# Performance work log

Hardware: AMD Instinct MI355X
Metric: run time of the kernel (lower is better)

The kernel has to match this reference:

```python
import jax, jax.numpy as jnp
import numpy as np

B, S, D, H = 2, 2048, 1024, 16
HD = D // H  # head_dim = 64


def setup_inputs() -> dict:
    key = jax.random.key(0)
    ks = jax.random.split(key, 12)
    scale = 1.0 / np.sqrt(D)
    inp = {
        "query": jax.random.normal(ks[0], (B, S, D), dtype=jnp.float32),
        "key_in": jax.random.normal(ks[1], (B, S, D), dtype=jnp.float32),
        "value": jax.random.normal(ks[2], (B, S, D), dtype=jnp.float32),
        "mask": jnp.zeros((B, S), dtype=bool),
        # nn.Linear weights stored as [out, in] like torch; y = x @ W.T + b
        "Wq": jax.random.normal(ks[3], (D, D), dtype=jnp.float32) * scale,
        "bq": jnp.zeros((D,), dtype=jnp.float32),
        "Wk": jax.random.normal(ks[4], (D, D), dtype=jnp.float32) * scale,
        "bk": jnp.zeros((D,), dtype=jnp.float32),
        "Wv": jax.random.normal(ks[5], (D, D), dtype=jnp.float32) * scale,
        "bv": jnp.zeros((D,), dtype=jnp.float32),
        "Wo": jax.random.normal(ks[6], (D, D), dtype=jnp.float32) * scale,
        "bo": jnp.zeros((D,), dtype=jnp.float32),
    }
    return inp


def reference(query, key_in, value, mask, Wq, bq, Wk, bk, Wv, bv, Wo, bo):
    def split_heads(x):  # [B,S,D] -> [B,H,S,HD]
        return x.reshape(B, -1, H, HD).transpose(0, 2, 1, 3)

    Q = split_heads(query @ Wq.T + bq)
    K = split_heads(key_in @ Wk.T + bk)
    V = split_heads(value @ Wv.T + bv)

    scores = jnp.einsum("bhqd,bhkd->bhqk", Q, K) / np.sqrt(HD)
    # key-padding mask: True -> -inf, broadcast over heads and query positions
    scores = jnp.where(mask[:, None, None, :], -jnp.inf, scores)
    attn = jax.nn.softmax(scores, axis=-1)
    out = jnp.einsum("bhqk,bhkd->bhqd", attn, V)  # [B,H,S,HD]
    out = out.transpose(0, 2, 1, 3).reshape(B, -1, D)
    return out @ Wo.T + bo
```

## Files before the change

### kernel.cpp

```cpp
#include <hip/hip_runtime.h>

typedef __attribute__((ext_vector_type(8))) __bf16 bf16x8;
typedef __attribute__((ext_vector_type(4))) float f32x4;
typedef __attribute__((ext_vector_type(16))) float f32x16;
typedef __attribute__((ext_vector_type(4))) unsigned int u32x4;
typedef __attribute__((ext_vector_type(8))) _Float16 f16x8;
typedef __attribute__((ext_vector_type(4))) _Float16 f16x4;
typedef unsigned short us;

#define SEQ 2048
#define DIM 1024
#define NH 16
#define HDIM 64

#define QSCALE 0.1803368801111204f

__device__ inline us f2bf(float f) {
    unsigned u = __builtin_bit_cast(unsigned, f);
    u += 0x7FFFu + ((u >> 16) & 1u);
    return (us)(u >> 16);
}

__device__ inline unsigned sx32(unsigned v) {
    return (unsigned)__shfl_xor((int)v, 32);
}

__device__ __forceinline__ void gload16(const us* g, us* l) {
    __builtin_amdgcn_global_load_lds(
        (const __attribute__((address_space(1))) unsigned int*)(const void*)g,
        (__attribute__((address_space(3))) unsigned int*)(void*)l, 16, 0, 0);
}

__global__ __launch_bounds__(256) void cast_many(
    const float* __restrict__ s0, const float* __restrict__ s1,
    const float* __restrict__ s2, const float* __restrict__ s3,
    us* __restrict__ dst, int n_each)
{
    const float* src = (blockIdx.y == 0) ? s0 : (blockIdx.y == 1) ? s1
                     : (blockIdx.y == 2) ? s2 : s3;
    size_t base = (size_t)blockIdx.y * (size_t)n_each;
    int i = (blockIdx.x * 256 + threadIdx.x) * 4;
    if (i < n_each) {
        float4 v = *(const float4*)(src + i);
        ushort4 o;
        o.x = f2bf(v.x); o.y = f2bf(v.y); o.z = f2bf(v.z); o.w = f2bf(v.w);
        *(ushort4*)(dst + base + i) = o;
    }
}

__global__ __launch_bounds__(64) void maskpack(
    const unsigned char* __restrict__ mask, unsigned* __restrict__ mw)
{
    int t = blockIdx.x * 64 + threadIdx.x;
    unsigned wv = 0;
#pragma unroll
    for (int j = 0; j < 32; j++) wv |= (mask[t * 32 + j] ? 1u : 0u) << j;
    mw[t] = wv;
}

#define BM 128
#define BN 128
#define BK 64

__device__ __forceinline__ void gemm_core(
    const us* __restrict__ A, const us* __restrict__ W,
    const float* __restrict__ bias, void* __restrict__ out,
    int M, int N, int K, int mode, float oscale)
{
    __shared__ us lA[BM * BK];
    __shared__ us lB[BN * BK];

    const int tid  = threadIdx.x;
    const int lane = tid & 63;
    const int w    = tid >> 6;
    const int wm   = w >> 1, wn = w & 1;
    const int m0   = blockIdx.y * BM, n0 = blockIdx.x * BN;
    const int g    = lane >> 4, li = lane & 15;

    const f32x4 fz = {0.f, 0.f, 0.f, 0.f};
    f32x4 acc[4][4];
#pragma unroll
    for (int i = 0; i < 4; i++)
#pragma unroll
        for (int j = 0; j < 4; j++) acc[i][j] = fz;

    for (int k0 = 0; k0 < K; k0 += BK) {
#pragma unroll
        for (int i = 0; i < 4; i++) {
            int v = tid + i * 256;
            int row = v >> 3, c8 = (v & 7) * 8;
            gload16(&A[(size_t)(m0 + row) * K + k0 + c8], &lA[v * 8]);
            gload16(&W[(size_t)(n0 + row) * K + k0 + c8], &lB[v * 8]);
        }
        __syncthreads();
#pragma unroll
        for (int kk = 0; kk < 2; kk++) {
            bf16x8 af[4], bfr[4];
#pragma unroll
            for (int i = 0; i < 4; i++)
                af[i] = *(const bf16x8*)&lA[(wm * 64 + i * 16 + li) * BK + kk * 32 + g * 8];
#pragma unroll
            for (int j = 0; j < 4; j++)
                bfr[j] = *(const bf16x8*)&lB[(wn * 64 + j * 16 + li) * BK + kk * 32 + g * 8];
#pragma unroll
            for (int i = 0; i < 4; i++)
#pragma unroll
                for (int j = 0; j < 4; j++)
                    acc[i][j] = __builtin_amdgcn_mfma_f32_16x16x32_bf16(
                        af[i], bfr[j], acc[i][j], 0, 0, 0);
        }
        __syncthreads();
    }

    const int r0 = g * 4;
#pragma unroll
    for (int i = 0; i < 4; i++) {
#pragma unroll
        for (int j = 0; j < 4; j++) {
            int col = n0 + wn * 64 + j * 16 + li;
            float bs = bias[col];
#pragma unroll
            for (int r = 0; r < 4; r++) {
                int row = m0 + wm * 64 + i * 16 + r0 + r;
                float val = (acc[i][j][r] + bs) * oscale;
                if (mode == 2) {
                    ((float*)out)[(size_t)row * N + col] = val;
                } else {
                    int b = row >> 11, s = row & (SEQ - 1);
                    int h = col >> 6, hd = col & (HDIM - 1);
                    size_t idx = (mode == 0)
                        ? ((((size_t)b * NH + h) * SEQ + s) * HDIM + hd)
                        : ((((size_t)b * NH + h) * HDIM + hd) * SEQ + s);
                    ((us*)out)[idx] = f2bf(val);
                }
            }
        }
    }
}

__global__ __launch_bounds__(256) void gemm_qkv(
    const us* __restrict__ xq, const us* __restrict__ xk, const us* __restrict__ xv,
    const us* __restrict__ wq, const us* __restrict__ wk, const us* __restrict__ wv,
    const float* __restrict__ bq, const float* __restrict__ bk, const float* __restrict__ bv,
    us* __restrict__ Qb, us* __restrict__ Kb, us* __restrict__ VTb)
{
    int z = blockIdx.z;
    if (z == 0)      gemm_core(xq, wq, bq, Qb,  2 * SEQ, DIM, DIM, 0, QSCALE);
    else if (z == 1) gemm_core(xk, wk, bk, Kb,  2 * SEQ, DIM, DIM, 0, 1.0f);
    else             gemm_core(xv, wv, bv, VTb, 2 * SEQ, DIM, DIM, 1, 1.0f);
}

__global__ __launch_bounds__(256) void gemm_one(
    const us* __restrict__ A, const us* __restrict__ W,
    const float* __restrict__ bias, float* __restrict__ out)
{
    gemm_core(A, W, bias, out, 2 * SEQ, DIM, DIM, 2, 1.0f);
}

__global__ __launch_bounds__(256, 4) void attn_split(
    const us* __restrict__ Qb, const us* __restrict__ Kb,
    const us* __restrict__ VT, const unsigned* __restrict__ mw,
    _Float16* __restrict__ opart, float* __restrict__ mlpart)
{
    const int tid  = threadIdx.x;
    const int w    = tid >> 6, lane = tid & 63;
    const int unit = blockIdx.x * 4 + w;
    const int tile = unit >> 1, half = unit & 1;
    const int bh   = tile >> 6, qt = tile & 63;
    const int b    = bh >> 4;
    const int q0   = qt * 32;
    const int ql   = lane & 31, hi = lane >> 5;
    const int kv0  = half * 1024, kv1 = kv0 + 1024;

    const us* Qp  = Qb + (((size_t)bh * SEQ) + q0 + ql) * HDIM + hi * 8;
    const us* Kp  = Kb + ((size_t)bh * SEQ + ql) * HDIM + hi * 8;
    const us* Vp0 = VT + ((size_t)bh * HDIM + ql) * SEQ + hi * 8;
    const us* Vp1 = Vp0 + 32 * SEQ;

    bf16x8 qf[4];
#pragma unroll
    for (int t = 0; t < 4; t++) qf[t] = *(const bf16x8*)(Qp + t * 16);

    const f32x16 z16 = {0,0,0,0,0,0,0,0,0,0,0,0,0,0,0,0};
    f32x16 o0 = z16, o1 = z16;
    float mrun = -1e30f, lrun = 0.f;

    bf16x8 kf[4];
#pragma unroll
    for (int t = 0; t < 4; t++) kf[t] = *(const bf16x8*)(Kp + (size_t)kv0 * HDIM + t * 16);

    for (int kv = kv0; kv < kv1; kv += 32) {
        f32x16 s = z16;
#pragma unroll
        for (int t = 0; t < 4; t++)
            s = __builtin_amdgcn_mfma_f32_32x32x16_bf16(kf[t], qf[t], s, 0, 0, 0);

        if (kv + 32 < kv1) {
            const us* Kn = Kp + (size_t)(kv + 32) * HDIM;
#pragma unroll
            for (int t = 0; t < 4; t++) kf[t] = *(const bf16x8*)(Kn + t * 16);
        }
        bf16x8 vf0[2], vf1[2];
#pragma unroll
        for (int t = 0; t < 2; t++) {
            vf0[t] = *(const bf16x8*)(Vp0 + kv + t * 16);
            vf1[t] = *(const bf16x8*)(Vp1 + kv + t * 16);
        }

        unsigned m32 = (unsigned)__builtin_amdgcn_readfirstlane(
            (int)mw[b * 64 + (kv >> 5)]);

        float t8[8];
#pragma unroll
        for (int j = 0; j < 8; j++) t8[j] = fmaxf(s[j], s[j + 8]);
#pragma unroll
        for (int j = 0; j < 4; j++) t8[j] = fmaxf(t8[j], t8[j + 4]);
        float pmax = fmaxf(fmaxf(t8[0], t8[1]), fmaxf(t8[2], t8[3]));

        if (!__all(pmax <= mrun + 8.f)) {
            float pm = fmaxf(pmax, __shfl_xor(pmax, 32));
            float nm = fmaxf(mrun, pm);
            float corr = __builtin_amdgcn_exp2f(mrun - nm);
            lrun *= corr;
#pragma unroll
            for (int j = 0; j < 16; j++) { o0[j] *= corr; o1[j] *= corr; }
            mrun = nm;
        }

        float p[16];
#pragma unroll
        for (int r = 0; r < 16; r++) p[r] = __builtin_amdgcn_exp2f(s[r] - mrun);
        if (m32) {
            unsigned ms = hi ? (m32 >> 4) : m32;
#pragma unroll
            for (int r = 0; r < 16; r++)
                if ((ms >> ((r & 3) + 8 * (r >> 2))) & 1) p[r] = 0.f;
        }
        float a8[8];
#pragma unroll
        for (int j = 0; j < 8; j++) a8[j] = p[j] + p[j + 8];
#pragma unroll
        for (int j = 0; j < 4; j++) a8[j] += a8[j + 4];
        lrun += (a8[0] + a8[1]) + (a8[2] + a8[3]);

        unsigned pw[8];
#pragma unroll
        for (int j = 0; j < 8; j++)
            asm("v_cvt_pk_bf16_f32 %0, %1, %2"
                : "=v"(pw[j]) : "v"(p[2 * j]), "v"(p[2 * j + 1]));

        unsigned y0 = sx32(hi ? pw[0] : pw[2]);
        unsigned y1 = sx32(hi ? pw[1] : pw[3]);
        unsigned y2 = sx32(hi ? pw[4] : pw[6]);
        unsigned y3 = sx32(hi ? pw[5] : pw[7]);

        u32x4 t0, t1;
        t0.x = hi ? y0    : pw[0];
        t0.y = hi ? y1    : pw[1];
        t0.z = hi ? pw[2] : y0;
        t0.w = hi ? pw[3] : y1;
        t1.x = hi ? y2    : pw[4];
        t1.y = hi ? y3    : pw[5];
        t1.z = hi ? pw[6] : y2;
        t1.w = hi ? pw[7] : y3;
        bf16x8 pa0 = __builtin_bit_cast(bf16x8, t0);
        bf16x8 pa1 = __builtin_bit_cast(bf16x8, t1);

        o0 = __builtin_amdgcn_mfma_f32_32x32x16_bf16(vf0[0], pa0, o0, 0, 0, 0);
        o0 = __builtin_amdgcn_mfma_f32_32x32x16_bf16(vf0[1], pa1, o0, 0, 0, 0);
        o1 = __builtin_amdgcn_mfma_f32_32x32x16_bf16(vf1[0], pa0, o1, 0, 0, 0);
        o1 = __builtin_amdgcn_mfma_f32_32x32x16_bf16(vf1[1], pa1, o1, 0, 0, 0);
    }

    float lh  = lrun + __shfl_xor(lrun, 32);
    float inv = __builtin_amdgcn_rcpf(lh);

    size_t orow = (size_t)half * 65536 + (size_t)bh * SEQ + q0 + ql;
    _Float16* od = opart + orow * 64;
#pragma unroll
    for (int g2 = 0; g2 < 4; g2++) {
        f16x4 v0, v1;
#pragma unroll
        for (int j = 0; j < 4; j++) {
            v0[j] = (_Float16)(o0[4 * g2 + j] * inv);
            v1[j] = (_Float16)(o1[4 * g2 + j] * inv);
        }
        *(f16x4*)(od + 8 * g2 + 4 * hi)      = v0;
        *(f16x4*)(od + 32 + 8 * g2 + 4 * hi) = v1;
    }
    if (hi == 0) {
        float2 mlv; mlv.x = mrun; mlv.y = lh;
        *(float2*)&mlpart[orow * 2] = mlv;
    }
}

__global__ __launch_bounds__(256) void attn_combine(
    const _Float16* __restrict__ op, const float* __restrict__ ml,
    us* __restrict__ AO)
{
    int t   = blockIdx.x * 256 + threadIdx.x;
    int row = t >> 3, dc = (t & 7) * 8;
    int bh  = row >> 11, q = row & (SEQ - 1);
    int b   = bh >> 4, h = bh & 15;

    float2 ml0 = *(const float2*)&ml[(size_t)row * 2];
    float2 ml1 = *(const float2*)&ml[(size_t)(65536 + row) * 2];
    float M  = fmaxf(ml0.x, ml1.x);
    float w0 = ml0.y * __builtin_amdgcn_exp2f(ml0.x - M);
    float w1 = ml1.y * __builtin_amdgcn_exp2f(ml1.x - M);
    float wi = __builtin_amdgcn_rcpf(w0 + w1);
    float a0 = w0 * wi, a1 = w1 * wi;

    f16x8 v0 = *(const f16x8*)(op + (size_t)row * 64 + dc);
    f16x8 v1 = *(const f16x8*)(op + 4194304 + (size_t)row * 64 + dc);

    ushort4 r0, r1;
    r0.x = f2bf(a0 * (float)v0[0] + a1 * (float)v1[0]);
    r0.y = f2bf(a0 * (float)v0[1] + a1 * (float)v1[1]);
    r0.z = f2bf(a0 * (float)v0[2] + a1 * (float)v1[2]);
    r0.w = f2bf(a0 * (float)v0[3] + a1 * (float)v1[3]);
    r1.x = f2bf(a0 * (float)v0[4] + a1 * (float)v1[4]);
    r1.y = f2bf(a0 * (float)v0[5] + a1 * (float)v1[5]);
    r1.z = f2bf(a0 * (float)v0[6] + a1 * (float)v1[6]);
    r1.w = f2bf(a0 * (float)v0[7] + a1 * (float)v1[7]);

    us* dst = AO + ((size_t)b * SEQ + q) * DIM + h * HDIM + dc;
    *(ushort4*)dst       = r0;
    *(ushort4*)(dst + 4) = r1;
}

extern "C" void kernel_launch(void* const* d_in, const int* in_sizes, int n_in,
                              void* d_out, int out_size, void* d_ws, size_t ws_size,
                              hipStream_t stream)
{
    const float* q  = (const float*)d_in[0];
    const float* k  = (const float*)d_in[1];
    const float* v  = (const float*)d_in[2];
    const unsigned char* mask = (const unsigned char*)d_in[3];
    const float* Wq = (const float*)d_in[4];
    const float* bq = (const float*)d_in[5];
    const float* Wk = (const float*)d_in[6];
    const float* bk = (const float*)d_in[7];
    const float* Wv = (const float*)d_in[8];
    const float* bv = (const float*)d_in[9];
    const float* Wo = (const float*)d_in[10];
    const float* bo = (const float*)d_in[11];

    us* ws  = (us*)d_ws;
    us* xq  = ws;
    us* xk  = ws + 4194304;
    us* xv  = ws + 8388608;
    us* wqb = ws + 12582912;
    us* wkb = ws + 13631488;
    us* wvb = ws + 14680064;
    us* wob = ws + 15728640;
    us* Qb  = ws + 16777216;
    us* Kb  = ws + 20971520;
    us* VTb = ws + 25165824;
    us* AO  = ws + 29360128;
    unsigned* mwords = (unsigned*)(ws + 33554432);
    _Float16* opart  = (_Float16*)ws;
    float*    mlpart = (float*)(ws + 8388608 + 524288);

    cast_many<<<dim3(4096, 3), 256, 0, stream>>>(q, k, v, q, xq, 4194304);
    cast_many<<<dim3(1024, 4), 256, 0, stream>>>(Wq, Wk, Wv, Wo, wqb, 1048576);
    maskpack<<<dim3(2), 64, 0, stream>>>(mask, mwords);

    gemm_qkv<<<dim3(DIM / BN, (2 * SEQ) / BM, 3), 256, 0, stream>>>(
        xq, xk, xv, wqb, wkb, wvb, bq, bk, bv, Qb, Kb, VTb);

    attn_split<<<dim3(1024), 256, 0, stream>>>(Qb, Kb, VTb, mwords, opart, mlpart);
    attn_combine<<<dim3(2048), 256, 0, stream>>>(opart, mlpart, AO);

    gemm_one<<<dim3(DIM / BN, (2 * SEQ) / BM), 256, 0, stream>>>(AO, wob, bo, (float*)d_out);
}
```

Baseline: 328.8 us.

## Store Q/K/V in MFMA-fragment tiled layout for contiguous attention loads

The QKV projection epilogue now writes Q, K and V^T in a blocked layout where each 32-row tile's MFMA operand fragments are contiguous per lane. The attention kernel then loads each fragment as a fully coalesced 1 KiB wave read instead of strided 16-byte reads across rows. This is meant to cut memory transactions and cache-line waste in the attention inner loop. The cost is more scattered scalar stores in the GEMM epilogue.

```diff
diff --git a/kernel.cpp b/kernel.cpp
--- a/kernel.cpp
+++ b/kernel.cpp
@@ -23,6 +23,15 @@
 
 __device__ inline unsigned sx32(unsigned v) {
     return (unsigned)__shfl_xor((int)v, 32);
+}
+
+__device__ __forceinline__ size_t qk_idx(int bh, int s, int d) {
+    return (((size_t)bh * 64 + (s >> 5)) << 11) + ((d >> 4) << 9)
+         + (((s & 31) + (((d >> 3) & 1) << 5)) << 3) + (d & 7);
+}
+__device__ __forceinline__ size_t v_idx(int bh, int d, int s) {
+    return (((size_t)bh * 64 + (s >> 5)) << 11) + ((((d >> 5) << 1) + ((s >> 4) & 1)) << 9)
+         + (((d & 31) + (((s >> 3) & 1) << 5)) << 3) + (s & 7);
 }
 
 __device__ __forceinline__ void gload16(const us* g, us* l) {
@@ -126,11 +135,10 @@
                 if (mode == 2) {
                     ((float*)out)[(size_t)row * N + col] = val;
                 } else {
-                    int b = row >> 11, s = row & (SEQ - 1);
-                    int h = col >> 6, hd = col & (HDIM - 1);
-                    size_t idx = (mode == 0)
-                        ? ((((size_t)b * NH + h) * SEQ + s) * HDIM + hd)
-                        : ((((size_t)b * NH + h) * HDIM + hd) * SEQ + s);
+                    int s = row & (SEQ - 1);
+                    int bh = ((row >> 11) << 4) + (col >> 6);
+                    int d  = col & (HDIM - 1);
+                    size_t idx = (mode == 0) ? qk_idx(bh, s, d) : v_idx(bh, d, s);
                     ((us*)out)[idx] = f2bf(val);
                 }
             }
@@ -172,14 +180,13 @@
     const int ql   = lane & 31, hi = lane >> 5;
     const int kv0  = half * 1024, kv1 = kv0 + 1024;
 
-    const us* Qp  = Qb + (((size_t)bh * SEQ) + q0 + ql) * HDIM + hi * 8;
-    const us* Kp  = Kb + ((size_t)bh * SEQ + ql) * HDIM + hi * 8;
-    const us* Vp0 = VT + ((size_t)bh * HDIM + ql) * SEQ + hi * 8;
-    const us* Vp1 = Vp0 + 32 * SEQ;
+    const us* Qf = Qb + (((size_t)bh * 64 + qt) << 11) + lane * 8;
+    const us* Kf = Kb + (((size_t)bh * 64) << 11) + lane * 8;
+    const us* Vf = VT + (((size_t)bh * 64) << 11) + lane * 8;
 
     bf16x8 qf[4];
 #pragma unroll
-    for (int t = 0; t < 4; t++) qf[t] = *(const bf16x8*)(Qp + t * 16);
+    for (int t = 0; t < 4; t++) qf[t] = *(const bf16x8*)(Qf + t * 512);
 
     const f32x16 z16 = {0,0,0,0,0,0,0,0,0,0,0,0,0,0,0,0};
     f32x16 o0 = z16, o1 = z16;
@@ -187,24 +194,27 @@
 
     bf16x8 kf[4];
 #pragma unroll
-    for (int t = 0; t < 4; t++) kf[t] = *(const bf16x8*)(Kp + (size_t)kv0 * HDIM + t * 16);
+    for (int t = 0; t < 4; t++)
+        kf[t] = *(const bf16x8*)(Kf + ((size_t)(kv0 >> 5) << 11) + t * 512);
 
     for (int kv = kv0; kv < kv1; kv += 32) {
+        const size_t koff = (size_t)(kv >> 5) << 11;
+
         f32x16 s = z16;
 #pragma unroll
         for (int t = 0; t < 4; t++)
             s = __builtin_amdgcn_mfma_f32_32x32x16_bf16(kf[t], qf[t], s, 0, 0, 0);
 
         if (kv + 32 < kv1) {
-            const us* Kn = Kp + (size_t)(kv + 32) * HDIM;
-#pragma unroll
-            for (int t = 0; t < 4; t++) kf[t] = *(const bf16x8*)(Kn + t * 16);
+            const us* Kn = Kf + koff + 2048;
+#pragma unroll
+            for (int t = 0; t < 4; t++) kf[t] = *(const bf16x8*)(Kn + t * 512);
         }
         bf16x8 vf0[2], vf1[2];
 #pragma unroll
         for (int t = 0; t < 2; t++) {
-            vf0[t] = *(const bf16x8*)(Vp0 + kv + t * 16);
-            vf1[t] = *(const bf16x8*)(Vp1 + kv + t * 16);
+            vf0[t] = *(const bf16x8*)(Vf + koff + t * 512);
+            vf1[t] = *(const bf16x8*)(Vf + koff + 1024 + t * 512);
         }
 
         unsigned m32 = (unsigned)__builtin_amdgcn_readfirstlane(
```

Result: faster. 263.7 us (-19.8%).
